# Optimization experiments

Hardware: AMD Instinct MI355X
Metric: run time of the kernel (lower is better)

## Reference

```python
import jax, jax.numpy as jnp
import numpy as np

N = 30000   # clients (single instance, repeat=1)
F = 16      # num_node_features
EP = 30000  # solution-graph (tour) edges per parent
EF = 240000 # full graph k-NN edges (degree 8)
H = 8       # heads
D = 64      # hidden_dim
R = 64      # routes per parent (= max_to_move)
HD = H * D  # 512


def _gatv2(x, src, dst, ea, Wl, Wr, We, att, b, d_out):
    # PyG GATv2Conv: score = att . leaky_relu(Wl x_src + Wr x_dst + We e), softmax over dst
    n = x.shape[0]
    xl = (x @ Wl).reshape(n, H, d_out)
    xr = (x @ Wr).reshape(n, H, d_out)
    ee = (ea @ We).reshape(-1, H, d_out)
    s = jax.nn.leaky_relu(xl[src] + xr[dst] + ee, 0.2)          # [E,H,d]
    logits = jnp.einsum('ehd,hd->eh', s, att)                    # [E,H]
    m = jax.ops.segment_max(logits, dst, num_segments=n)
    ex = jnp.exp(logits - m[dst])
    den = jax.ops.segment_sum(ex, dst, num_segments=n)
    alpha = ex / (den[dst] + 1e-16)
    out = jax.ops.segment_sum(xl[src] * alpha[..., None], dst, num_segments=n)
    return out.reshape(n, H * d_out) + b


def _bn(x, g, b):
    # BatchNorm with track_running_stats=False -> batch statistics
    mu = jnp.mean(x, 0)
    v = jnp.var(x, 0)
    return (x - mu) * jax.lax.rsqrt(v + 1e-5) * g + b


def _routes(emb, rid):
    # sum client embeddings per route, then prefix sums over routes (moved vs kept sets)
    rs = jax.ops.segment_sum(emb, rid, num_segments=R)   # [R, 2HD]
    cs = jnp.cumsum(rs, 0)
    return cs, cs[-1] - cs


def setup_inputs() -> dict:
    key = jax.random.key(0)
    ks = iter(jax.random.split(key, 64))
    sc = 0.05
    rn = lambda shape: jax.random.normal(next(ks), shape, jnp.float32)
    d = {}
    d['x_p1'] = rn((N, F)); d['x_p2'] = rn((N, F)); d['x_full'] = rn((N, F))
    d['ea_p1'] = jax.random.uniform(next(ks), (EP, 1))
    d['ea_p2'] = jax.random.uniform(next(ks), (EP, 1))
    d['ea_full'] = jax.random.uniform(next(ks), (EF, 1))
    d['ei_p1'] = jax.random.randint(next(ks), (2, EP), 0, N)
    d['ei_p2'] = jax.random.randint(next(ks), (2, EP), 0, N)
    d['ei_full'] = jax.random.randint(next(ks), (2, EF), 0, N)
    d['route_p1'] = jax.random.randint(next(ks), (N,), 0, R)
    d['route_p2'] = jax.random.randint(next(ks), (N,), 0, R)
    # GAT params: (SolutionGraph, FullGraph, both)
    for tag, cin, dout in (('1', F, D), ('2', F, D), ('3', 2 * HD, 2 * D)):
        d['Wl' + tag] = rn((cin, H * dout)) * sc
        d['Wr' + tag] = rn((cin, H * dout)) * sc
        d['We' + tag] = rn((1, H * dout)) * sc
        d['att' + tag] = rn((H, dout)) * sc
        d['b' + tag] = jnp.zeros((H * dout,), jnp.float32)
    d['bng'] = jnp.ones((2 * HD,), jnp.float32); d['bnb'] = jnp.zeros((2 * HD,), jnp.float32)
    d['png'] = jnp.ones((8 * HD,), jnp.float32); d['pnb'] = jnp.zeros((8 * HD,), jnp.float32)
    dims = [8 * HD, 4 * HD, 2 * HD, HD, HD // 2, HD // 4, HD // 8, HD // 16, 1]
    for i in range(8):
        d['W%d' % (i + 1)] = rn((dims[i], dims[i + 1])) * sc
        d['c%d' % (i + 1)] = jnp.zeros((dims[i + 1],), jnp.float32)
    return d


def reference(x_p1, x_p2, x_full, ea_p1, ea_p2, ea_full, ei_p1, ei_p2, ei_full,
              route_p1, route_p2,
              Wl1, Wr1, We1, att1, b1, Wl2, Wr2, We2, att2, b2,
              Wl3, Wr3, We3, att3, b3, bng, bnb, png, pnb,
              W1, c1, W2, c2, W3, c3, W4, c4, W5, c5, W6, c6, W7, c7, W8, c8):
    p1 = _gatv2(x_p1, ei_p1[0], ei_p1[1], ea_p1, Wl1, Wr1, We1, att1, b1, D)
    p2 = _gatv2(x_p2, ei_p2[0], ei_p2[1], ea_p2, Wl1, Wr1, We1, att1, b1, D)
    fg = _gatv2(x_full, ei_full[0], ei_full[1], ea_full, Wl2, Wr2, We2, att2, b2, D)
    # single instance -> repeat=1: concat client embedding with full-graph embedding
    p1f = _bn(jnp.concatenate([p1, fg], 1), bng, bnb)
    p2f = _bn(jnp.concatenate([p2, fg], 1), bng, bnb)
    p1f = _gatv2(p1f, ei_p1[0], ei_p1[1], ea_p1, Wl3, Wr3, We3, att3, b3, 2 * D)
    p2f = _gatv2(p2f, ei_p2[0], ei_p2[1], ea_p2, Wl3, Wr3, We3, att3, b3, 2 * D)
    c1s, r1s = _routes(p1f, route_p1)
    c2s, r2s = _routes(p2f, route_p2)
    ptop = jnp.concatenate([c1s, r1s, c2s, r2s], 1)   # [R, 8*HD]
    h = _bn(ptop, png, pnb)
    lrelu = lambda z: jax.nn.leaky_relu(z, 0.01)
    h = lrelu(h @ W1 + c1)
    h = lrelu(h @ W2 + c2)
    h = lrelu(h @ W3 + c3)
    h = lrelu(h @ W4 + c4)
    h = lrelu(h @ W5 + c5)
    h = lrelu(h @ W6 + c6)
    h = lrelu(h @ W7 + c7)
    h = h @ W8 + c8
    probs = jax.nn.sigmoid(h).ravel()
    ptop_batch = jnp.zeros((R,), jnp.int32)
    return probs, ptop_batch
```

## Files before the change

### kernel.cpp

```cpp
#include <hip/hip_runtime.h>
#include <stdint.h>

typedef unsigned short u16;
typedef unsigned int   u32;
typedef __attribute__((ext_vector_type(8))) short bf16x8;
typedef __attribute__((ext_vector_type(4))) float f32x4;

#define NN    30000
#define EFULL 240000
#define EPAR  30000

__device__ __forceinline__ float b2f(u16 u){ u32 x=((u32)u)<<16; float f; __builtin_memcpy(&f,&x,4); return f; }
__device__ __forceinline__ u16 f2b(float f){ u32 x; __builtin_memcpy(&x,&f,4); x += 0x7fffu + ((x>>16)&1u); return (u16)(x>>16); }

__device__ __forceinline__ void gload_lds16(const u16* g, u16* l){
  __builtin_amdgcn_global_load_lds((const __attribute__((address_space(1))) void*)g,
                                   (__attribute__((address_space(3))) void*)l, 16, 0, 0);
}

__global__ void k_fail(float* out){ int t=threadIdx.x; if(t<128) out[t]=2.0f; }

__global__ void k_counte3(const int* __restrict__ d0, const int* __restrict__ d1, const int* __restrict__ d2,
                          int* __restrict__ c0, int* __restrict__ c1, int* __restrict__ c2){
  int z = blockIdx.z;
  const int* d = z==0? d0 : z==1? d1 : d2;
  int* c = z==0? c0 : z==1? c1 : c2;
  int E = z==0? EFULL : EPAR;
  int e = blockIdx.x*256 + threadIdx.x;
  if (e < E) atomicAdd(&c[d[e]], 1);
}

__global__ void k_scan3(const int* __restrict__ c0, const int* __restrict__ c1, const int* __restrict__ c2,
                        int* __restrict__ r0, int* __restrict__ r1, int* __restrict__ r2,
                        int* __restrict__ w0, int* __restrict__ w1, int* __restrict__ w2){
  __shared__ int sums[1024];
  int z = blockIdx.x;
  const int* cnt = z==0? c0 : z==1? c1 : c2;
  int* rp = z==0? r0 : z==1? r1 : r2;
  int* wp = z==0? w0 : z==1? w1 : w2;
  int t = threadIdx.x;
  const int CH = (NN + 1023)/1024;
  int c00 = t*CH;
  int s = 0;
  for (int i=0;i<CH;i++){ int idx=c00+i; s += (idx<NN)? cnt[idx] : 0; }
  sums[t] = s; __syncthreads();
  for (int off=1; off<1024; off<<=1){
    int v = (t>=off)? sums[t-off] : 0;
    __syncthreads();
    sums[t] += v;
    __syncthreads();
  }
  int run = (t==0)? 0 : sums[t-1];
  for (int i=0;i<CH;i++){
    int idx=c00+i;
    if (idx<NN){ rp[idx]=run; wp[idx]=run; run += cnt[idx]; }
  }
  if (t==1023) rp[NN] = sums[1023];
}

__global__ void k_fill3(const int* __restrict__ d0, const int* __restrict__ d1, const int* __restrict__ d2,
                        int* __restrict__ w0, int* __restrict__ w1, int* __restrict__ w2,
                        int* __restrict__ x0, int* __restrict__ x1, int* __restrict__ x2){
  int z = blockIdx.z;
  const int* d = z==0? d0 : z==1? d1 : d2;
  int* w = z==0? w0 : z==1? w1 : w2;
  int* x = z==0? x0 : z==1? x1 : x2;
  int E = z==0? EFULL : EPAR;
  int e = blockIdx.x*256 + threadIdx.x;
  if (e < E){ int p = atomicAdd(&w[d[e]], 1); x[p] = e; }
}

__global__ void k_count64(const int* __restrict__ rt0, const int* __restrict__ rt1,
                          const int* __restrict__ d0, const int* __restrict__ d1,
                          int* __restrict__ c0, int* __restrict__ c1,
                          int* __restrict__ c2, int* __restrict__ c3){
  int z = blockIdx.z;
  int i = blockIdx.x*256 + threadIdx.x;
  if (i >= NN) return;
  if      (z==0) atomicAdd(&c0[rt0[i]], 1);
  else if (z==1) atomicAdd(&c1[rt1[i]], 1);
  else if (z==2) atomicAdd(&c2[rt0[d0[i]]], 1);
  else           atomicAdd(&c3[rt1[d1[i]]], 1);
}

__global__ void k_scan64x4(const int* __restrict__ c0, const int* __restrict__ c1,
                           const int* __restrict__ c2, const int* __restrict__ c3,
                           int* __restrict__ r0, int* __restrict__ r1,
                           int* __restrict__ r2, int* __restrict__ r3,
                           int* __restrict__ w2, int* __restrict__ w3){
  int t = threadIdx.x;
  if (t >= 4) return;
  const int* c = t==0?c0:t==1?c1:t==2?c2:c3;
  int* r = t==0?r0:t==1?r1:t==2?r2:r3;
  int run=0;
  for (int i=0;i<64;i++){
    r[i]=run;
    if (t==2) w2[i]=run;
    if (t==3) w3[i]=run;
    run+=c[i];
  }
  r[64]=run;
}

__global__ void k_fille2(const int* __restrict__ rt0, const int* __restrict__ rt1,
                         const int* __restrict__ d0, const int* __restrict__ d1,
                         int* __restrict__ w2, int* __restrict__ w3,
                         int* __restrict__ x2, int* __restrict__ x3){
  int z = blockIdx.z;
  int i = blockIdx.x*256 + threadIdx.x;
  if (i >= EPAR) return;
  if (z==0){ int p=atomicAdd(&w2[rt0[d0[i]]],1);  x2[p]=i; }
  else     { int p=atomicAdd(&w3[rt1[d1[i]]],1);  x3[p]=i; }
}

__global__ void k_nre(const int* __restrict__ rp1, const int* __restrict__ rp2,
                      const int* __restrict__ rt1, const int* __restrict__ rt2,
                      int* __restrict__ n1, int* __restrict__ n2){
  int z = blockIdx.z;
  int n = blockIdx.x*256 + threadIdx.x;
  if (n >= NN) return;
  if (z==0){ if (rp1[n+1] > rp1[n]) atomicAdd(&n1[rt1[n]], 1); }
  else     { if (rp2[n+1] > rp2[n]) atomicAdd(&n2[rt2[n]], 1); }
}

__global__ __launch_bounds__(256) void k_xwl(const float* __restrict__ x,
                                             const float* __restrict__ Wl, u16* __restrict__ xl){
  int n = blockIdx.x;
  int c = blockIdx.y*256 + threadIdx.x;
  float a=0.f;
  #pragma unroll
  for (int k=0;k<16;k++) a += x[n*16+k]*Wl[k*512+c];
  xl[(size_t)n*512+c]=f2b(a);
}

__global__ __launch_bounds__(256) void k_gat1f(const int* __restrict__ ei,
    const float* __restrict__ ea,
    const int* __restrict__ rp, const int* __restrict__ eix,
    const float* __restrict__ x, const float* __restrict__ Wr,
    const float* __restrict__ We, const float* __restrict__ att,
    const u16* __restrict__ xl,
    const float* __restrict__ bias, u16* __restrict__ out){
  int lane = threadIdx.x & 63;
  int n = blockIdx.x*4 + (threadIdx.x>>6);
  if (n >= NN) return;
  int j0 = lane*8;
  float xv[16];
  #pragma unroll
  for (int k=0;k<16;k++) xv[k] = x[n*16+k];
  float we8[8], at8[8], rv8[8];
  #pragma unroll
  for (int j=0;j<8;j++){
    we8[j]=We[j0+j]; at8[j]=att[j0+j];
    float s=0.f;
    #pragma unroll
    for (int k=0;k<16;k++) s += xv[k]*Wr[k*512 + j0 + j];
    rv8[j]=s;
  }
  int r0 = rp[n], r1 = rp[n+1];
  float den = 0.f;
  float acc[8] = {0,0,0,0,0,0,0,0};
  for (int i=r0;i<r1;i++){
    int e = eix[i];
    int src = ei[e];
    float eaw = ea[e];
    bf16x8 lv = *(const bf16x8*)(xl + (size_t)src*512 + j0);
    float lvf[8];
    float logit = 0.f;
    #pragma unroll
    for (int j=0;j<8;j++){
      lvf[j] = b2f((u16)lv[j]);
      float v = lvf[j] + rv8[j] + eaw*we8[j];
      v = v>0.f? v : 0.2f*v;
      logit += v*at8[j];
    }
    logit += __shfl_xor(logit,1);
    logit += __shfl_xor(logit,2);
    logit += __shfl_xor(logit,4);
    float a = __expf(logit);
    den += a;
    #pragma unroll
    for (int j=0;j<8;j++) acc[j] += a*lvf[j];
  }
  float inv = 1.f/(den + 1e-16f);
  #pragma unroll
  for (int j=0;j<8;j++) out[(size_t)n*512 + j0 + j] = f2b(acc[j]*inv + bias[j0+j]);
}

__global__ __launch_bounds__(256) void k_bnstats(const u16* __restrict__ P1, const u16* __restrict__ P2,
    const u16* __restrict__ PF, float* __restrict__ s1, float* __restrict__ s2, float* __restrict__ sF){
  int z = blockIdx.y;
  const u16* P = z==0? P1 : z==1? P2 : PF;
  float* st = z==0? s1 : z==1? s2 : sF;
  int t = threadIdx.x;
  const u32* Pu = (const u32*)P;
  int r0 = blockIdx.x*250, r1 = r0+250;
  float a0=0.f,a1=0.f,q0=0.f,q1=0.f;
  for (int r=r0;r<r1;r++){
    u32 v = Pu[(size_t)r*256 + t];
    float a = b2f((u16)(v & 0xffffu));
    float b = b2f((u16)(v >> 16));
    a0+=a; q0+=a*a; a1+=b; q1+=b*b;
  }
  atomicAdd(&st[2*t],       a0);
  atomicAdd(&st[2*t+1],     a1);
  atomicAdd(&st[512+2*t],   q0);
  atomicAdd(&st[512+2*t+1], q1);
}

__global__ void k_prep(const float* __restrict__ st1, const float* __restrict__ st2,
                       const float* __restrict__ stF,
                       const float* __restrict__ g, const float* __restrict__ b,
                       float* __restrict__ sc1, float* __restrict__ sh1,
                       float* __restrict__ sc2, float* __restrict__ sh2){
  int k = blockIdx.x*256 + threadIdx.x;
  if (k >= 1024) return;
  const float invN = 1.f/30000.f;
  const float* st = (k<512)? st1 : stF;
  int kk = k & 511;
  float mu = st[kk]*invN;
  float var = st[512+kk]*invN - mu*mu;
  float sc = g[k]*rsqrtf(var + 1e-5f);
  sc1[k] = sc; sh1[k] = b[k] - mu*sc;
  st = (k<512)? st2 : stF;
  mu = st[kk]*invN;
  var = st[512+kk]*invN - mu*mu;
  sc = g[k]*rsqrtf(var + 1e-5f);
  sc2[k] = sc; sh2[k] = b[k] - mu*sc;
}

__global__ __launch_bounds__(256) void k_bt(const float* __restrict__ B0, const float* __restrict__ B1,
                                            const float* __restrict__ sc1, const float* __restrict__ sc2,
                                            u16* __restrict__ Bt1, u16* __restrict__ Bt2){
  __shared__ float tile[64][65];
  int bk = blockIdx.x;
  int bn = blockIdx.y;
  int par = blockIdx.z>>1, half = blockIdx.z&1;
  const float* B = half ? B1 : B0;
  const float* sc = par ? sc2 : sc1;
  u16* Bt = par ? Bt2 : Bt1;
  int nb = half*1024;
  for (int i = threadIdx.x; i < 64*64; i += 256){
    int r = i>>6, c = i&63;
    tile[c][r] = B[(size_t)(bk*64+r)*1024 + bn*64 + c] * sc[bk*64+r];
  }
  __syncthreads();
  for (int i = threadIdx.x; i < 64*64; i += 256){
    int r = i>>6, c = i&63;
    Bt[(size_t)(nb + bn*64 + r)*1024 + bk*64 + c] = f2b(tile[r][c]);
  }
}

__global__ void k_shiftb(const float* __restrict__ B0, const float* __restrict__ B1,
                         const float* __restrict__ sh1, const float* __restrict__ sh2,
                         float* __restrict__ sb1, float* __restrict__ sb2){
  int c = blockIdx.x*256 + threadIdx.x;
  const float* sh = blockIdx.y ? sh2 : sh1;
  float* sb = blockIdx.y ? sb2 : sb1;
  const float* B = (c < 1024) ? B0 : B1;
  int cc = c & 1023;
  float s = 0.f;
  for (int k=0;k<1024;k++) s += sh[k]*B[(size_t)k*1024 + cc];
  sb[c] = s;
}

__global__ __launch_bounds__(256) void k_gemm(const u16* __restrict__ A0, const u16* __restrict__ A1,
    const u16* __restrict__ Bt, u16* __restrict__ C, int M){
  __shared__ u16 As[128*64];
  __shared__ u16 Bs[128*64];
  int lin = blockIdx.y*16 + blockIdx.x;
  int wg  = (lin&7)*470 + (lin>>3);
  int n0 = (wg & 15)*128;
  int m0 = (wg >> 4)*128;
  int t = threadIdx.x;
  int wave = t>>6, lane = t&63;
  int wm = (wave>>1)*64, wn = (wave&1)*64;
  int rr = lane&15, kq = (lane>>4)*8;
  int srow = t>>3;
  int scol = (t&7)*8;
  int ssw  = ((t&7) ^ (srow&7))*8;
  f32x4 acc[4][4];
  #pragma unroll
  for (int m=0;m<4;m++)
    #pragma unroll
    for (int n=0;n<4;n++){ acc[m][n][0]=0.f; acc[m][n][1]=0.f; acc[m][n][2]=0.f; acc[m][n][3]=0.f; }
  for (int k0=0; k0<1024; k0+=64){
    const u16* Ap = (k0 < 512) ? A0 : A1;
    int kc = k0 & 511;
    #pragma unroll
    for (int i=0;i<4;i++){
      int row = i*32 + srow;
      gload_lds16(Ap + (size_t)(m0+row)*512 + kc + ssw, As + row*64 + scol);
    }
    #pragma unroll
    for (int i=0;i<4;i++){
      int row = i*32 + srow;
      gload_lds16(Bt + (size_t)(n0+row)*1024 + k0 + ssw, Bs + row*64 + scol);
    }
    __syncthreads();
    #pragma unroll
    for (int ks=0; ks<2; ks++){
      int pc = ((ks*4 + (lane>>4)) ^ (lane&7))*8;
      bf16x8 af[4], bb[4];
      #pragma unroll
      for (int m=0;m<4;m++) af[m] = *(const bf16x8*)(&As[(wm + m*16 + rr)*64 + pc]);
      #pragma unroll
      for (int n=0;n<4;n++) bb[n] = *(const bf16x8*)(&Bs[(wn + n*16 + rr)*64 + pc]);
      #pragma unroll
      for (int m=0;m<4;m++)
        #pragma unroll
        for (int n=0;n<4;n++)
          acc[m][n] = __builtin_amdgcn_mfma_f32_16x16x32_bf16(af[m], bb[n], acc[m][n], 0, 0, 0);
    }
    __syncthreads();
  }
  int rq = (lane>>4)*4;
  #pragma unroll
  for (int m=0;m<4;m++)
    #pragma unroll
    for (int n=0;n<4;n++)
      #pragma unroll
      for (int j=0;j<4;j++){
        int row = m0 + wm + m*16 + rq + j;
        int col = n0 + wn + n*16 + rr;
        if (row < M) C[(size_t)row*2048 + col] = f2b(acc[m][n][j]);
      }
}

__global__ __launch_bounds__(256) void k_edge2f(const int* __restrict__ ei,
    const float* __restrict__ ea,
    const int* __restrict__ rp, const int* __restrict__ eix,
    const float* __restrict__ We, const float* __restrict__ att,
    const u16* __restrict__ CAT, const float* __restrict__ sb,
    float* __restrict__ alpha){
  int lane = threadIdx.x & 63;
  int n = blockIdx.x*4 + (threadIdx.x>>6);
  if (n >= NN) return;
  int j0 = lane*16;
  float rv[16], we16[16], at16[16];
  bf16x8 rr0 = *(const bf16x8*)(CAT + (size_t)n*2048 + 1024 + j0);
  bf16x8 rr1 = *(const bf16x8*)(CAT + (size_t)n*2048 + 1024 + j0 + 8);
  #pragma unroll
  for (int j=0;j<16;j++){
    rv[j] = b2f((u16)((j<8)? rr0[j] : rr1[j-8])) + sb[1024+j0+j] + sb[j0+j];
    we16[j]=We[j0+j]; at16[j]=att[j0+j];
  }
  int e0 = rp[n], e1 = rp[n+1];
  float den = 0.f;
  for (int i=e0;i<e1;i++){
    int e = eix[i];
    int src = ei[e];
    float eaw = ea[e];
    bf16x8 l0 = *(const bf16x8*)(CAT + (size_t)src*2048 + j0);
    bf16x8 l1 = *(const bf16x8*)(CAT + (size_t)src*2048 + j0 + 8);
    float logit = 0.f;
    #pragma unroll
    for (int j=0;j<16;j++){
      float v = b2f((u16)((j<8)? l0[j] : l1[j-8])) + rv[j] + eaw*we16[j];
      v = v>0.f? v : 0.2f*v;
      logit += v*at16[j];
    }
    logit += __shfl_xor(logit,1);
    logit += __shfl_xor(logit,2);
    logit += __shfl_xor(logit,4);
    float ex_ = __expf(logit);
    if ((lane&7)==0){ alpha[(size_t)e*8 + (lane>>3)] = ex_; den += ex_; }
  }
  float dh = __shfl(den, (lane&7)*8);
  float inv = 1.f/(dh + 1e-16f);
  if (lane < 8){
    for (int i=e0;i<e1;i++){
      int e = eix[i];
      alpha[(size_t)e*8 + lane] *= inv;
    }
  }
}

#define ECH 32
__global__ __launch_bounds__(256) void k_agg2pool(const int* __restrict__ ei,
    const int* __restrict__ rerp, const int* __restrict__ reix,
    const int* __restrict__ rrp, const int* __restrict__ nre,
    const float* __restrict__ alpha, const u16* __restrict__ CAT,
    const float* __restrict__ b3, const float* __restrict__ sb,
    float* __restrict__ rs){
  int r = blockIdx.x;
  int c = blockIdx.z*256 + threadIdx.x;
  int h = c >> 7;
  int i0 = rerp[r], i1 = rerp[r+1];
  int per = (i1 - i0 + ECH - 1)/ECH;
  int s0 = i0 + blockIdx.y*per;
  int s1 = min(i1, s0 + per);
  float acc = 0.f;
  for (int i=s0;i<s1;i++){
    int e = reix[i];
    float a = alpha[(size_t)e*8 + h];
    acc += a * b2f(CAT[(size_t)ei[e]*2048 + c]);
  }
  if (blockIdx.y == 0)
    acc += (float)(rrp[r+1]-rrp[r]) * b3[c] + (float)nre[r] * sb[c];
  if (s0 < s1 || blockIdx.y == 0) atomicAdd(&rs[r*1024 + c], acc);
}

__global__ void k_cumsum_bn(const float* __restrict__ rs1, const float* __restrict__ rs2,
                            const float* __restrict__ g, const float* __restrict__ b,
                            float* __restrict__ h){
  const float* rs = blockIdx.y ? rs2 : rs1;
  int colbase = blockIdx.y ? 2048 : 0;
  int c = blockIdx.x*256 + threadIdx.x;
  float tot = 0.f;
  for (int r=0;r<64;r++) tot += rs[r*1024+c];
  float cs=0.f, s0=0.f,q0=0.f,s1=0.f,q1=0.f;
  for (int r=0;r<64;r++){
    cs += rs[r*1024+c];
    float m = tot - cs;
    s0+=cs; q0+=cs*cs; s1+=m; q1+=m*m;
  }
  float mu0=s0*(1.f/64.f), v0=q0*(1.f/64.f)-mu0*mu0, n0=rsqrtf(v0+1e-5f);
  float mu1=s1*(1.f/64.f), v1=q1*(1.f/64.f)-mu1*mu1, n1=rsqrtf(v1+1e-5f);
  float g0=g[colbase+c],      b0=b[colbase+c];
  float g1=g[colbase+1024+c], b1=b[colbase+1024+c];
  cs = 0.f;
  for (int r=0;r<64;r++){
    cs += rs[r*1024+c];
    float m = tot - cs;
    h[r*4096 + colbase + c]        = (cs-mu0)*n0*g0 + b0;
    h[r*4096 + colbase + 1024 + c] = (m -mu1)*n1*g1 + b1;
  }
}

#define KC 512
__global__ __launch_bounds__(256) void k_mlp_part(const float* __restrict__ In,
    const float* __restrict__ W, float* __restrict__ PART, int Ci, int Co){
  __shared__ float tin[64*64];
  int c  = blockIdx.x*64 + (threadIdx.x&63);
  int rg = threadIdx.x>>6;
  int k0 = blockIdx.y*KC, k1 = min(Ci, k0+KC);
  float acc[16];
  #pragma unroll
  for (int j=0;j<16;j++) acc[j]=0.f;
  for (int ks=k0; ks<k1; ks+=64){
    int kw = min(64, k1-ks);
    __syncthreads();
    for (int i=threadIdx.x;i<64*64;i+=256){
      int r=i>>6, k=i&63;
      tin[i] = (k<kw)? In[(size_t)r*Ci + ks + k] : 0.f;
    }
    __syncthreads();
    if (c < Co){
      for (int k=0;k<kw;k+=4){
        float4 w4;
        w4.x = W[(size_t)(ks+k  )*Co + c];
        w4.y = W[(size_t)(ks+k+1)*Co + c];
        w4.z = W[(size_t)(ks+k+2)*Co + c];
        w4.w = W[(size_t)(ks+k+3)*Co + c];
        #pragma unroll
        for (int j=0;j<16;j++){
          float4 t4 = *(const float4*)(&tin[(rg*16+j)*64 + k]);
          acc[j] += t4.x*w4.x + t4.y*w4.y + t4.z*w4.z + t4.w*w4.w;
        }
      }
    }
  }
  if (c < Co){
    float* P = PART + (size_t)blockIdx.y*64*Co;
    #pragma unroll
    for (int j=0;j<16;j++)
      P[(size_t)(rg*16+j)*Co + c] = acc[j];
  }
}

__global__ void k_mlp_red(const float* __restrict__ PART, const float* __restrict__ bias,
                          float* __restrict__ Out, int Co, int SK, int act){
  int idx = blockIdx.x*256 + threadIdx.x;
  if (idx >= 64*Co) return;
  int c = idx % Co;
  float s = bias[c];
  for (int sk=0; sk<SK; sk++) s += PART[(size_t)sk*64*Co + idx];
  if (act) s = s>0.f ? s : 0.01f*s;
  Out[idx] = s;
}

__global__ __launch_bounds__(256) void k_mlp_tail(const float* __restrict__ In,
    const float* __restrict__ W6, const float* __restrict__ c6,
    const float* __restrict__ W7, const float* __restrict__ c7,
    const float* __restrict__ W8, const float* __restrict__ c8,
    float* __restrict__ out){
  __shared__ float A[64*128];
  __shared__ float B[64*64];
  int t = threadIdx.x;
  for (int i=t;i<64*128;i+=256) A[i] = In[i];
  __syncthreads();
  for (int idx=t; idx<64*64; idx+=256){
    int r=idx>>6, c=idx&63;
    float s=c6[c];
    for (int k=0;k<128;k++) s += A[r*128+k]*W6[k*64+c];
    B[idx] = s>0.f? s : 0.01f*s;
  }
  __syncthreads();
  for (int idx=t; idx<64*32; idx+=256){
    int r=idx>>5, c=idx&31;
    float s=c7[c];
    for (int k=0;k<64;k++) s += B[r*64+k]*W7[k*32+c];
    A[idx] = s>0.f? s : 0.01f*s;
  }
  __syncthreads();
  if (t<64){
    float s=c8[0];
    for (int k=0;k<32;k++) s += A[t*32+k]*W8[k];
    out[t] = 1.f/(1.f + __expf(-s));
    out[64+t] = 0.f;
  }
}

extern "C" void kernel_launch(void* const* d_in, const int* in_sizes, int n_in,
                              void* d_out, int out_size, void* d_ws, size_t ws_size,
                              hipStream_t stream)
{
  const float* x_p1   = (const float*)d_in[0];
  const float* x_p2   = (const float*)d_in[1];
  const float* x_full = (const float*)d_in[2];
  const float* ea_p1  = (const float*)d_in[3];
  const float* ea_p2  = (const float*)d_in[4];
  const float* ea_full= (const float*)d_in[5];
  const int* ei_p1  = (const int*)d_in[6];
  const int* ei_p2  = (const int*)d_in[7];
  const int* ei_full= (const int*)d_in[8];
  const int* route_p1 = (const int*)d_in[9];
  const int* route_p2 = (const int*)d_in[10];
  const float *Wl1=(const float*)d_in[11], *Wr1=(const float*)d_in[12], *We1=(const float*)d_in[13], *att1=(const float*)d_in[14], *b1=(const float*)d_in[15];
  const float *Wl2=(const float*)d_in[16], *Wr2=(const float*)d_in[17], *We2=(const float*)d_in[18], *att2=(const float*)d_in[19], *b2=(const float*)d_in[20];
  const float *Wl3=(const float*)d_in[21], *Wr3=(const float*)d_in[22], *We3=(const float*)d_in[23], *att3=(const float*)d_in[24], *b3=(const float*)d_in[25];
  const float *bng=(const float*)d_in[26], *bnb=(const float*)d_in[27], *png=(const float*)d_in[28], *pnb=(const float*)d_in[29];
  const float *W[8], *Cb[8];
  for (int i=0;i<8;i++){ W[i]=(const float*)d_in[30+2*i]; Cb[i]=(const float*)d_in[31+2*i]; }

  char* w = (char*)d_ws;
  size_t off = 0;
  auto alloc = [&](size_t bytes)->char*{ char* p = w + off; off += (bytes + 255) & ~(size_t)255; return p; };
  u16* P1bf = (u16*)alloc((size_t)NN*512*2);
  u16* P2bf = (u16*)alloc((size_t)NN*512*2);
  u16* FGbf = (u16*)alloc((size_t)NN*512*2);
  char* BIG = alloc((size_t)NN*2048*2);
  u16*   XLbf = (u16*)BIG;
  u16*   CATbf= (u16*)BIG;
  u16*   Bt1  = (u16*)alloc((size_t)2048*1024*2);
  u16*   Bt2  = (u16*)alloc((size_t)2048*1024*2);
  float* ALPHA=(float*)alloc((size_t)EPAR*8*4);
  float* st1 = (float*)alloc(1024*4);
  float* st2 = (float*)alloc(1024*4);
  float* stF = (float*)alloc(1024*4);
  float* rs1 = (float*)alloc(64*1024*4);
  float* rs2 = (float*)alloc(64*1024*4);
  float* sc1 = (float*)alloc(1024*4);
  float* sh1 = (float*)alloc(1024*4);
  float* sc2 = (float*)alloc(1024*4);
  float* sh2 = (float*)alloc(1024*4);
  float* sb1 = (float*)alloc(2048*4);
  float* sb2 = (float*)alloc(2048*4);
  float* H0  = (float*)alloc(64*4096*4);
  float* H1  = (float*)alloc(64*4096*4);
  float* PART= (float*)alloc((size_t)8*64*2048*4);
  char* cnt_base = alloc(0);
  int* cntF = (int*)alloc(NN*4);
  int* cntA = (int*)alloc(NN*4);
  int* cntB = (int*)alloc(NN*4);
  int* c64a = (int*)alloc(64*4);
  int* c64b = (int*)alloc(64*4);
  int* c64c = (int*)alloc(64*4);
  int* c64d = (int*)alloc(64*4);
  int* nre1 = (int*)alloc(64*4);
  int* nre2 = (int*)alloc(64*4);
  size_t cnt_bytes = (size_t)((char*)alloc(0) - cnt_base);
  int* wpF = (int*)alloc(NN*4);
  int* wpA = (int*)alloc(NN*4);
  int* wpB = (int*)alloc(NN*4);
  int* w64c= (int*)alloc(64*4);
  int* w64d= (int*)alloc(64*4);
  int* rpF = (int*)alloc((NN+1)*4);
  int* rp1 = (int*)alloc((NN+1)*4);
  int* rp2 = (int*)alloc((NN+1)*4);
  int* eixF= (int*)alloc((size_t)EFULL*4);
  int* eix1= (int*)alloc((size_t)EPAR*4);
  int* eix2= (int*)alloc((size_t)EPAR*4);
  int* rr1 = (int*)alloc(65*4);
  int* rr2 = (int*)alloc(65*4);
  int* rerp1=(int*)alloc(65*4);
  int* rerp2=(int*)alloc(65*4);
  int* reix1=(int*)alloc((size_t)EPAR*4);
  int* reix2=(int*)alloc((size_t)EPAR*4);
  if (ws_size < off){ k_fail<<<1,128,0,stream>>>((float*)d_out); return; }

  hipMemsetAsync(cnt_base, 0, cnt_bytes, stream);
  hipMemsetAsync(st1, 0, (size_t)((char*)rs2 - (char*)st1) + 64*1024*4, stream);

  k_counte3<<<dim3((EFULL+255)/256,1,3), 256, 0, stream>>>(ei_full+EFULL, ei_p1+EPAR, ei_p2+EPAR,
                                                           cntF, cntA, cntB);
  k_scan3  <<<3, 1024, 0, stream>>>(cntF, cntA, cntB, rpF, rp1, rp2, wpF, wpA, wpB);
  k_fill3  <<<dim3((EFULL+255)/256,1,3), 256, 0, stream>>>(ei_full+EFULL, ei_p1+EPAR, ei_p2+EPAR,
                                                           wpF, wpA, wpB, eixF, eix1, eix2);
  k_count64<<<dim3((NN+255)/256,1,4), 256, 0, stream>>>(route_p1, route_p2, ei_p1+EPAR, ei_p2+EPAR,
                                                        c64a, c64b, c64c, c64d);
  k_scan64x4<<<1, 64, 0, stream>>>(c64a,c64b,c64c,c64d, rr1,rr2,rerp1,rerp2, w64c,w64d);
  k_fille2 <<<dim3((NN+255)/256,1,2), 256, 0, stream>>>(route_p1, route_p2, ei_p1+EPAR, ei_p2+EPAR,
                                                        w64c, w64d, reix1, reix2);
  k_nre    <<<dim3((NN+255)/256,1,2), 256, 0, stream>>>(rp1, rp2, route_p1, route_p2, nre1, nre2);

  auto gat1 = [&](const float* x, const int* ei, const float* ea, const int* rp, const int* eix,
                  const float* Wl, const float* Wr, const float* We, const float* att, const float* bias,
                  u16* out){
    k_xwl  <<<dim3(NN,2), 256, 0, stream>>>(x, Wl, XLbf);
    k_gat1f<<<(NN+3)/4, 256, 0, stream>>>(ei, ea, rp, eix, x, Wr, We, att, XLbf, bias, out);
  };
  gat1(x_full, ei_full, ea_full, rpF, eixF, Wl2, Wr2, We2, att2, b2, FGbf);
  gat1(x_p1,   ei_p1,   ea_p1,   rp1, eix1, Wl1, Wr1, We1, att1, b1, P1bf);
  gat1(x_p2,   ei_p2,   ea_p2,   rp2, eix2, Wl1, Wr1, We1, att1, b1, P2bf);

  k_bnstats<<<dim3(120,3), 256, 0, stream>>>(P1bf, P2bf, FGbf, st1, st2, stF);
  k_prep   <<<4, 256, 0, stream>>>(st1, st2, stF, bng, bnb, sc1, sh1, sc2, sh2);
  k_bt     <<<dim3(16,16,4), 256, 0, stream>>>(Wl3, Wr3, sc1, sc2, Bt1, Bt2);
  k_shiftb <<<dim3(8,2), 256, 0, stream>>>(Wl3, Wr3, sh1, sh2, sb1, sb2);

  auto layer2 = [&](const u16* Pbf, const u16* Bt, const float* sb,
                    const int* ei, const float* ea, const int* rp, const int* eix,
                    const int* rrp, const int* nre, const int* rerp, const int* reix, float* rs){
    k_gemm <<<dim3(16, (NN+127)/128), 256, 0, stream>>>(Pbf, FGbf, Bt, CATbf, NN);
    k_edge2f<<<(NN+3)/4, 256, 0, stream>>>(ei, ea, rp, eix, We3, att3, CATbf, sb, ALPHA);
    k_agg2pool<<<dim3(64,ECH,4), 256, 0, stream>>>(ei, rerp, reix, rrp, nre, ALPHA, CATbf, b3, sb, rs);
  };
  layer2(P1bf, Bt1, sb1, ei_p1, ea_p1, rp1, eix1, rr1, nre1, rerp1, reix1, rs1);
  layer2(P2bf, Bt2, sb2, ei_p2, ea_p2, rp2, eix2, rr2, nre2, rerp2, reix2, rs2);

  k_cumsum_bn<<<dim3(4,2), 256, 0, stream>>>(rs1, rs2, png, pnb, H0);

  int dims[9] = {4096, 2048, 1024, 512, 256, 128, 64, 32, 1};
  float* bufs[2] = {H0, H1};
  for (int i=0;i<5;i++){
    int Ci = dims[i], Co = dims[i+1];
    int SK = (Ci + KC - 1)/KC;
    k_mlp_part<<<dim3((Co+63)/64, SK), 256, 0, stream>>>(bufs[i&1], W[i], PART, Ci, Co);
    k_mlp_red <<<(64*Co+255)/256, 256, 0, stream>>>(PART, Cb[i], bufs[(i+1)&1], Co, SK, 1);
  }
  k_mlp_tail<<<1, 256, 0, stream>>>(bufs[1], W[5], Cb[5], W[6], Cb[6], W[7], Cb[7], (float*)d_out);
}
```

Measured before the change: 1.714 ms.

## Replace layer-2 GEMM with 256x256-tile double-buffered 8-wave pipelined kernel

Rewrites the layer-2 bf16 GEMM to use 256x256 output tiles with 512 threads (8 waves), double-buffered LDS staging via global_load_lds, and interleaving of next-tile loads with MFMA work under explicit vmcnt waits and s_setprio. The aim is to hide global-load latency behind compute and to raise arithmetic intensity per tile. The input buffers are padded to 30208 rows so the larger tiles can read past N without a bounds check. The LDS footprint grows to 128KB per block, which lowers occupancy, and the hand-placed waitcnt counts must match the load order exactly.

```diff
diff --git a/kernel.cpp b/kernel.cpp
--- a/kernel.cpp
+++ b/kernel.cpp
@@ -7,6 +7,7 @@
 typedef __attribute__((ext_vector_type(4))) float f32x4;
 
 #define NN    30000
+#define NNP   30208
 #define EFULL 240000
 #define EPAR  30000
 
@@ -263,59 +264,146 @@
   sb[c] = s;
 }
 
-__global__ __launch_bounds__(256) void k_gemm(const u16* __restrict__ A0, const u16* __restrict__ A1,
+__global__ __launch_bounds__(512) void k_gemm8(const u16* __restrict__ A0, const u16* __restrict__ A1,
     const u16* __restrict__ Bt, u16* __restrict__ C, int M){
-  __shared__ u16 As[128*64];
-  __shared__ u16 Bs[128*64];
-  int lin = blockIdx.y*16 + blockIdx.x;
-  int wg  = (lin&7)*470 + (lin>>3);
-  int n0 = (wg & 15)*128;
-  int m0 = (wg >> 4)*128;
+  __shared__ u16 Asm[2][256*64];
+  __shared__ u16 Bsm[2][256*64];
+  int lin = blockIdx.y*8 + blockIdx.x;
+  int wg  = (lin&7)*118 + (lin>>3);
+  int n0 = (wg & 7)*256;
+  int m0 = (wg >> 3)*256;
   int t = threadIdx.x;
   int wave = t>>6, lane = t&63;
-  int wm = (wave>>1)*64, wn = (wave&1)*64;
-  int rr = lane&15, kq = (lane>>4)*8;
+  int wm = (wave>>2)*128;
+  int wn = (wave&3)*64;
+  int rr = lane&15;
+  int kq = lane>>4;
   int srow = t>>3;
-  int scol = (t&7)*8;
-  int ssw  = ((t&7) ^ (srow&7))*8;
-  f32x4 acc[4][4];
+  int schunk = t&7;
+  int ssw = schunk ^ (srow&7);
+
+  f32x4 acc[8][4];
   #pragma unroll
-  for (int m=0;m<4;m++)
+  for (int m=0;m<8;m++)
     #pragma unroll
     for (int n=0;n<4;n++){ acc[m][n][0]=0.f; acc[m][n][1]=0.f; acc[m][n][2]=0.f; acc[m][n][3]=0.f; }
-  for (int k0=0; k0<1024; k0+=64){
-    const u16* Ap = (k0 < 512) ? A0 : A1;
-    int kc = k0 & 511;
+
+  auto stageA = [&](int db, int kt, int R0){
+    const u16* Ap = (kt < 8) ? A0 : A1;
+    int kc = (kt & 7)*64;
+    int row = R0 + srow;
+    gload_lds16(Ap + (size_t)(m0+row)*512 + kc + ssw*8, &Asm[db][row*64 + schunk*8]);
+  };
+  auto stageB = [&](int db, int kt, int R0){
+    int row = R0 + srow;
+    gload_lds16(Bt + (size_t)(n0+row)*1024 + kt*64 + ssw*8, &Bsm[db][row*64 + schunk*8]);
+  };
+  auto rdA = [&](int db, int m, int ks)->bf16x8{
+    int row = wm + m*16 + rr;
+    int pc = (ks*4 + kq) ^ (row & 7);
+    return *(const bf16x8*)(&Asm[db][row*64 + pc*8]);
+  };
+  auto rdB = [&](int db, int n, int ks)->bf16x8{
+    int row = wn + n*16 + rr;
+    int pc = (ks*4 + kq) ^ (row & 7);
+    return *(const bf16x8*)(&Bsm[db][row*64 + pc*8]);
+  };
+
+  stageB(0,0,0); stageB(0,0,64); stageB(0,0,128); stageB(0,0,192);
+  stageA(0,0,0); stageA(0,0,128);
+  stageA(0,0,64); stageA(0,0,192);
+
+  const int NT = 16;
+  for (int kt=0; kt<NT; ++kt){
+    int db = kt & 1, nb = db ^ 1;
+    bool more = (kt < NT-1);
+    asm volatile("s_waitcnt vmcnt(2)" ::: "memory");
+    __builtin_amdgcn_s_barrier();
+    __builtin_amdgcn_sched_barrier(0);
+
+    if (more){ stageB(nb, kt+1, 0); stageB(nb, kt+1, 64); }
+    bf16x8 bb[2][4];
     #pragma unroll
-    for (int i=0;i<4;i++){
-      int row = i*32 + srow;
-      gload_lds16(Ap + (size_t)(m0+row)*512 + kc + ssw, As + row*64 + scol);
-    }
-    #pragma unroll
-    for (int i=0;i<4;i++){
-      int row = i*32 + srow;
-      gload_lds16(Bt + (size_t)(n0+row)*1024 + k0 + ssw, Bs + row*64 + scol);
-    }
-    __syncthreads();
-    #pragma unroll
-    for (int ks=0; ks<2; ks++){
-      int pc = ((ks*4 + (lane>>4)) ^ (lane&7))*8;
-      bf16x8 af[4], bb[4];
-      #pragma unroll
-      for (int m=0;m<4;m++) af[m] = *(const bf16x8*)(&As[(wm + m*16 + rr)*64 + pc]);
-      #pragma unroll
-      for (int n=0;n<4;n++) bb[n] = *(const bf16x8*)(&Bs[(wn + n*16 + rr)*64 + pc]);
-      #pragma unroll
-      for (int m=0;m<4;m++)
-        #pragma unroll
-        for (int n=0;n<4;n++)
-          acc[m][n] = __builtin_amdgcn_mfma_f32_16x16x32_bf16(af[m], bb[n], acc[m][n], 0, 0, 0);
-    }
-    __syncthreads();
-  }
+    for (int ks=0;ks<2;ks++)
+      #pragma unroll
+      for (int n=0;n<4;n++) bb[ks][n] = rdB(db, n, ks);
+    {
+      bf16x8 af[2][2];
+      #pragma unroll
+      for (int mi=0;mi<2;mi++)
+        #pragma unroll
+        for (int ks=0;ks<2;ks++) af[mi][ks] = rdA(db, mi, ks);
+      __builtin_amdgcn_s_setprio(1);
+      #pragma unroll
+      for (int mi=0;mi<2;mi++)
+        #pragma unroll
+        for (int n=0;n<4;n++){
+          acc[mi][n] = __builtin_amdgcn_mfma_f32_16x16x32_bf16(af[mi][0], bb[0][n], acc[mi][n], 0,0,0);
+          acc[mi][n] = __builtin_amdgcn_mfma_f32_16x16x32_bf16(af[mi][1], bb[1][n], acc[mi][n], 0,0,0);
+        }
+      __builtin_amdgcn_s_setprio(0);
+    }
+    if (more){ stageB(nb, kt+1, 128); stageB(nb, kt+1, 192); }
+    {
+      bf16x8 af[2][2];
+      #pragma unroll
+      for (int mi=0;mi<2;mi++)
+        #pragma unroll
+        for (int ks=0;ks<2;ks++) af[mi][ks] = rdA(db, 2+mi, ks);
+      __builtin_amdgcn_s_setprio(1);
+      #pragma unroll
+      for (int mi=0;mi<2;mi++)
+        #pragma unroll
+        for (int n=0;n<4;n++){
+          acc[2+mi][n] = __builtin_amdgcn_mfma_f32_16x16x32_bf16(af[mi][0], bb[0][n], acc[2+mi][n], 0,0,0);
+          acc[2+mi][n] = __builtin_amdgcn_mfma_f32_16x16x32_bf16(af[mi][1], bb[1][n], acc[2+mi][n], 0,0,0);
+        }
+      __builtin_amdgcn_s_setprio(0);
+    }
+    if (kt == NT-1) asm volatile("s_waitcnt vmcnt(0)" ::: "memory");
+    else            asm volatile("s_waitcnt vmcnt(4)" ::: "memory");
+    __builtin_amdgcn_s_barrier();
+    __builtin_amdgcn_sched_barrier(0);
+
+    if (more){ stageA(nb, kt+1, 0); stageA(nb, kt+1, 128); }
+    {
+      bf16x8 af[2][2];
+      #pragma unroll
+      for (int mi=0;mi<2;mi++)
+        #pragma unroll
+        for (int ks=0;ks<2;ks++) af[mi][ks] = rdA(db, 4+mi, ks);
+      __builtin_amdgcn_s_setprio(1);
+      #pragma unroll
+      for (int mi=0;mi<2;mi++)
+        #pragma unroll
+        for (int n=0;n<4;n++){
+          acc[4+mi][n] = __builtin_amdgcn_mfma_f32_16x16x32_bf16(af[mi][0], bb[0][n], acc[4+mi][n], 0,0,0);
+          acc[4+mi][n] = __builtin_amdgcn_mfma_f32_16x16x32_bf16(af[mi][1], bb[1][n], acc[4+mi][n], 0,0,0);
+        }
+      __builtin_amdgcn_s_setprio(0);
+    }
+    if (more){ stageA(nb, kt+1, 64); stageA(nb, kt+1, 192); }
+    {
+      bf16x8 af[2][2];
+      #pragma unroll
+      for (int mi=0;mi<2;mi++)
+        #pragma unroll
+        for (int ks=0;ks<2;ks++) af[mi][ks] = rdA(db, 6+mi, ks);
+      __builtin_amdgcn_s_setprio(1);
+      #pragma unroll
+      for (int mi=0;mi<2;mi++)
+        #pragma unroll
+        for (int n=0;n<4;n++){
+          acc[6+mi][n] = __builtin_amdgcn_mfma_f32_16x16x32_bf16(af[mi][0], bb[0][n], acc[6+mi][n], 0,0,0);
+          acc[6+mi][n] = __builtin_amdgcn_mfma_f32_16x16x32_bf16(af[mi][1], bb[1][n], acc[6+mi][n], 0,0,0);
+        }
+      __builtin_amdgcn_s_setprio(0);
+    }
+  }
+
   int rq = (lane>>4)*4;
   #pragma unroll
-  for (int m=0;m<4;m++)
+  for (int m=0;m<8;m++)
     #pragma unroll
     for (int n=0;n<4;n++)
       #pragma unroll
@@ -536,9 +624,9 @@
   char* w = (char*)d_ws;
   size_t off = 0;
   auto alloc = [&](size_t bytes)->char*{ char* p = w + off; off += (bytes + 255) & ~(size_t)255; return p; };
-  u16* P1bf = (u16*)alloc((size_t)NN*512*2);
-  u16* P2bf = (u16*)alloc((size_t)NN*512*2);
-  u16* FGbf = (u16*)alloc((size_t)NN*512*2);
+  u16* P1bf = (u16*)alloc((size_t)NNP*512*2);
+  u16* P2bf = (u16*)alloc((size_t)NNP*512*2);
+  u16* FGbf = (u16*)alloc((size_t)NNP*512*2);
   char* BIG = alloc((size_t)NN*2048*2);
   u16*   XLbf = (u16*)BIG;
   u16*   CATbf= (u16*)BIG;
@@ -622,7 +710,7 @@
   auto layer2 = [&](const u16* Pbf, const u16* Bt, const float* sb,
                     const int* ei, const float* ea, const int* rp, const int* eix,
                     const int* rrp, const int* nre, const int* rerp, const int* reix, float* rs){
-    k_gemm <<<dim3(16, (NN+127)/128), 256, 0, stream>>>(Pbf, FGbf, Bt, CATbf, NN);
+    k_gemm8 <<<dim3(8, 118), 512, 0, stream>>>(Pbf, FGbf, Bt, CATbf, NN);
     k_edge2f<<<(NN+3)/4, 256, 0, stream>>>(ei, ea, rp, eix, We3, att3, CATbf, sb, ALPHA);
     k_agg2pool<<<dim3(64,ECH,4), 256, 0, stream>>>(ei, rerp, reix, rrp, nre, ALPHA, CATbf, b3, sb, rs);
   };
```

After: 1.763 ms (median of 2 runs). +2.9%, slower.
